# Kernel tuning notes

Hardware: AMD Instinct MI355X
Metric: run time of the kernel (lower is better)

Reference implementation:

```python
import jax, jax.numpy as jnp
import numpy as np
import math

B, S, D = 2, 2048, 2048
H, KV, HD = 32, 8, 64
G = H // KV  # 4
BASE = 10000.0


def _rope_tables(seq_len, dtype):
    inv_freq = 1.0 / (BASE ** (jnp.arange(0, HD, 2, dtype=jnp.float32) / HD))
    t = jnp.arange(seq_len, dtype=jnp.float32)
    freqs = jnp.outer(t, inv_freq)               # [S, HD/2]
    emb = jnp.concatenate([freqs, freqs], -1)     # [S, HD]
    return jnp.cos(emb).astype(dtype), jnp.sin(emb).astype(dtype)


def _rotate_half(x):
    x1, x2 = x[..., : HD // 2], x[..., HD // 2 :]
    return jnp.concatenate([-x2, x1], axis=-1)


def setup_inputs() -> dict:
    key = jax.random.key(0)
    ks = jax.random.split(key, 5)
    s = 0.02
    return {
        "hidden_states": jax.random.normal(ks[0], (B, S, D), jnp.float32),
        "Wq": jax.random.normal(ks[1], (D, H * HD), jnp.float32) * s,
        "Wk": jax.random.normal(ks[2], (D, KV * HD), jnp.float32) * s,
        "Wv": jax.random.normal(ks[3], (D, KV * HD), jnp.float32) * s,
        "Wo": jax.random.normal(ks[4], (D, D), jnp.float32) * s,
    }


def reference(hidden_states, Wq, Wk, Wv, Wo):
    b, s, _ = hidden_states.shape
    q = (hidden_states @ Wq).reshape(b, s, H, HD).transpose(0, 2, 1, 3)   # [B,H,S,HD]
    k = (hidden_states @ Wk).reshape(b, s, KV, HD).transpose(0, 2, 1, 3)  # [B,KV,S,HD]
    v = (hidden_states @ Wv).reshape(b, s, KV, HD).transpose(0, 2, 1, 3)

    cos, sin = _rope_tables(s, hidden_states.dtype)  # [S, HD]
    cos = cos[None, None]
    sin = sin[None, None]
    q = q * cos + _rotate_half(q) * sin
    k = k * cos + _rotate_half(k) * sin

    # GQA: repeat kv heads to match query heads
    k = jnp.repeat(k, G, axis=1)  # [B,H,S,HD]
    v = jnp.repeat(v, G, axis=1)

    scores = jnp.einsum("bhqd,bhkd->bhqk", q, k) / math.sqrt(HD)
    causal = jnp.triu(jnp.full((s, s), float("-inf"), dtype=scores.dtype), k=1)
    scores = scores + causal
    attn = jax.nn.softmax(scores, axis=-1)
    out = jnp.einsum("bhqk,bhkd->bhqd", attn, v)          # [B,H,S,HD]
    out = out.transpose(0, 2, 1, 3).reshape(b, s, H * HD)  # [B,S,D]
    return out @ Wo
```

## Files before the change

kernel.cpp:

```cpp
#include <hip/hip_runtime.h>
#include <hip/hip_bf16.h>

#define BATCH  2
#define SEQ    2048
#define DMODEL 2048
#define NHEADS 32
#define NKV    8
#define HDIM   64
#define ROWS   (BATCH * SEQ)
#define NQKV   3072

typedef __attribute__((ext_vector_type(8))) short bf16x8;
typedef __attribute__((ext_vector_type(4))) float floatx4;

__device__ __forceinline__ float b2f(unsigned short u) {
    union { unsigned int i; float f; } x; x.i = ((unsigned int)u) << 16; return x.f;
}
__device__ __forceinline__ unsigned short f2b(float f) {
    union { float f; unsigned int i; } x; x.f = f;
    unsigned int r = x.i + 0x7fffu + ((x.i >> 16) & 1u);
    return (unsigned short)(r >> 16);
}
__device__ __forceinline__ unsigned int pkbf(float a, float b) {
    union { __hip_bfloat162 h; unsigned int u; } x;
    x.h = __float22bfloat162_rn(make_float2(a, b));
    return x.u;
}

#define GLD16(g, l) __builtin_amdgcn_global_load_lds( \
    (const __attribute__((address_space(1))) unsigned int*)(g), \
    (__attribute__((address_space(3))) unsigned int*)(l), 16, 0, 0)

template <bool BF16_OUT>
__global__ __launch_bounds__(256) void mfma_gemm(const unsigned short* __restrict__ A,
                                                 const unsigned short* __restrict__ Bt,
                                                 void* __restrict__ Cout,
                                                 int M, int N, int K) {
    __shared__ unsigned short As[128 * 32];
    __shared__ unsigned short Bs[128 * 32];

    const int tid  = threadIdx.x;
    const int wave = tid >> 6;
    const int lane = tid & 63;
    const int m0 = blockIdx.y * 128;
    const int n0 = blockIdx.x * 128;
    const int wr0 = (wave >> 1) * 64;
    const int wc0 = (wave & 1) * 64;

    const int srow = wave * 32 + (lane >> 2);
    const int skc  = (lane & 3) * 8;
    const unsigned short* Ap0 = A  + (size_t)(m0 + srow) * K + skc;
    const unsigned short* Ap1 = Ap0 + (size_t)16 * K;
    const unsigned short* Bp0 = Bt + (size_t)(n0 + srow) * K + skc;
    const unsigned short* Bp1 = Bp0 + (size_t)16 * K;
    unsigned short* Al0 = &As[wave * 1024];
    unsigned short* Al1 = &As[wave * 1024 + 512];
    unsigned short* Bl0 = &Bs[wave * 1024];
    unsigned short* Bl1 = &Bs[wave * 1024 + 512];

    const int fr = lane & 15;
    const int fk = (lane >> 4) * 8;

    floatx4 acc[4][4];
    #pragma unroll
    for (int r = 0; r < 4; ++r)
        #pragma unroll
        for (int c = 0; c < 4; ++c)
            #pragma unroll
            for (int g = 0; g < 4; ++g) acc[r][c][g] = 0.f;

    for (int k0 = 0; k0 < K; k0 += 32) {
        __syncthreads();
        GLD16(Ap0 + k0, Al0);
        GLD16(Ap1 + k0, Al1);
        GLD16(Bp0 + k0, Bl0);
        GLD16(Bp1 + k0, Bl1);
        __syncthreads();

        bf16x8 af[4], bfr[4];
        #pragma unroll
        for (int r = 0; r < 4; ++r)
            af[r] = *(const bf16x8*)&As[(wr0 + r * 16 + fr) * 32 + fk];
        #pragma unroll
        for (int c = 0; c < 4; ++c)
            bfr[c] = *(const bf16x8*)&Bs[(wc0 + c * 16 + fr) * 32 + fk];
        #pragma unroll
        for (int r = 0; r < 4; ++r)
            #pragma unroll
            for (int c = 0; c < 4; ++c)
                acc[r][c] = __builtin_amdgcn_mfma_f32_16x16x32_bf16(af[r], bfr[c], acc[r][c], 0, 0, 0);
    }

    const int erow = (lane >> 4) * 4;
    const int ecol = lane & 15;
    #pragma unroll
    for (int r = 0; r < 4; ++r)
        #pragma unroll
        for (int c = 0; c < 4; ++c)
            #pragma unroll
            for (int g = 0; g < 4; ++g) {
                int row = m0 + wr0 + r * 16 + erow + g;
                int col = n0 + wc0 + c * 16 + ecol;
                if (BF16_OUT)
                    ((unsigned short*)Cout)[(size_t)row * N + col] = f2b(acc[r][c][g]);
                else
                    ((float*)Cout)[(size_t)row * N + col] = acc[r][c][g];
            }
}

__global__ __launch_bounds__(256) void transpose_cast_all(const float* __restrict__ Wq,
                                                          const float* __restrict__ Wk,
                                                          const float* __restrict__ Wv,
                                                          const float* __restrict__ Wo,
                                                          unsigned short* __restrict__ Wt,
                                                          unsigned short* __restrict__ Wot) {
    __shared__ float t[32][33];
    int bx = blockIdx.x;
    const float* src; unsigned short* dst; int N, nb;
    if (bx < 64)      { src = Wq; dst = Wt;                          N = 2048; nb = bx; }
    else if (bx < 80) { src = Wk; dst = Wt + (size_t)2048 * DMODEL;  N = 512;  nb = bx - 64; }
    else if (bx < 96) { src = Wv; dst = Wt + (size_t)2560 * DMODEL;  N = 512;  nb = bx - 80; }
    else              { src = Wo; dst = Wot;                         N = 2048; nb = bx - 96; }
    const int n0 = nb * 32, k0 = blockIdx.y * 32;
    const int tx = threadIdx.x & 31, ty = threadIdx.x >> 5;
    #pragma unroll
    for (int i = 0; i < 32; i += 8)
        t[ty + i][tx] = src[(size_t)(k0 + ty + i) * N + n0 + tx];
    __syncthreads();
    #pragma unroll
    for (int i = 0; i < 32; i += 8)
        dst[(size_t)(n0 + ty + i) * DMODEL + k0 + tx] = f2b(t[tx][ty + i]);
}

__global__ void cast_f32_to_bf16(const float* __restrict__ src,
                                 unsigned short* __restrict__ dst, int n) {
    int i = (blockIdx.x * 256 + threadIdx.x) * 8;
    if (i >= n) return;
    float4 a = *(const float4*)(src + i);
    float4 b = *(const float4*)(src + i + 4);
    uint4 o;
    o.x = pkbf(a.x, a.y); o.y = pkbf(a.z, a.w);
    o.z = pkbf(b.x, b.y); o.w = pkbf(b.z, b.w);
    *(uint4*)(dst + i) = o;
}

__global__ void rope_all(unsigned short* __restrict__ buf) {
    int idx = blockIdx.x * blockDim.x + threadIdx.x;
    int i   = idx & 31;
    int tmp = idx >> 5;
    int hh  = tmp % 40;
    int row = tmp / 40;
    if (row >= ROWS) return;
    float scale = (hh < 32) ? 0.125f : 1.0f;
    int t = row & (SEQ - 1);
    float inv_freq = powf(10000.0f, -(float)i * (1.0f / 32.0f));
    float ang = (float)t * inv_freq;
    float s, c;
    sincosf(ang, &s, &c);
    unsigned short* p = buf + (size_t)row * NQKV + hh * 64 + i;
    float x1 = b2f(p[0]), x2 = b2f(p[32]);
    p[0]  = f2b((x1 * c - x2 * s) * scale);
    p[32] = f2b((x2 * c + x1 * s) * scale);
}

__global__ __launch_bounds__(256, 4) void attn_mfma(const unsigned short* __restrict__ QKV,
                                                    unsigned short* __restrict__ Ctx) {
    __shared__ unsigned short Ks[64][72];
    __shared__ unsigned short Vts[64][72];
    __shared__ unsigned short Ps[4][32][72];

    const int tid  = threadIdx.x;
    const int wave = tid >> 6;
    const int lane = tid & 63;
    const int px = blockIdx.x;
    const int h  = blockIdx.y;
    const int b  = blockIdx.z;
    const int kvh = h >> 2;

    const int fr = lane & 15;
    const int fg = lane >> 4;
    const size_t base = (size_t)(b * SEQ) * NQKV;

    const int krow = tid >> 2, kc0 = (tid & 3) * 16;
    const int vp2 = tid & 31, vh0 = (tid >> 5) * 8;
    const unsigned short* kbase = QKV + base + (size_t)krow * NQKV + 2048 + kvh * HDIM + kc0;
    const unsigned short* vbase = QKV + base + (size_t)(2 * vp2) * NQKV + 2560 + kvh * HDIM + vh0;

    #pragma unroll 1
    for (int t = 0; t < 2; ++t) {
        const int qb = (t == 0) ? (15 - px) : px;
        const int wbase = qb * 128 + wave * 32;

        bf16x8 qf[2][2];
        #pragma unroll
        for (int rg = 0; rg < 2; ++rg)
            #pragma unroll
            for (int ks = 0; ks < 2; ++ks)
                qf[rg][ks] = *(const bf16x8*)(QKV + base + (size_t)(wbase + rg * 16 + fr) * NQKV
                                              + h * HDIM + ks * 32 + fg * 8);

        float l[2];
        floatx4 acc[4][2];
        #pragma unroll
        for (int rg = 0; rg < 2; ++rg) l[rg] = 0.f;
        #pragma unroll
        for (int j2 = 0; j2 < 4; ++j2)
            #pragma unroll
            for (int rg = 0; rg < 2; ++rg)
                #pragma unroll
                for (int g = 0; g < 4; ++g) acc[j2][rg][g] = 0.f;

        const int nkb = 2 * qb + 2;

        bf16x8 kr0 = *(const bf16x8*)kbase;
        bf16x8 kr1 = *(const bf16x8*)(kbase + 8);
        bf16x8 v0  = *(const bf16x8*)vbase;
        bf16x8 v1  = *(const bf16x8*)(vbase + NQKV);

        for (int kb = 0; kb < nkb; ++kb) {
            __syncthreads();
            *(bf16x8*)&Ks[krow][kc0]     = kr0;
            *(bf16x8*)&Ks[krow][kc0 + 8] = kr1;
            #pragma unroll
            for (int j = 0; j < 8; ++j) {
                unsigned int w = (unsigned int)(unsigned short)v0[j]
                               | ((unsigned int)(unsigned short)v1[j] << 16);
                *(unsigned int*)&Vts[vh0 + j][2 * vp2] = w;
            }
            {
                int nx = (kb + 1 < nkb) ? kb + 1 : kb;
                const unsigned short* kp = kbase + (size_t)(nx * 64) * NQKV;
                const unsigned short* vp = vbase + (size_t)(nx * 64) * NQKV;
                kr0 = *(const bf16x8*)kp;
                kr1 = *(const bf16x8*)(kp + 8);
                v0  = *(const bf16x8*)vp;
                v1  = *(const bf16x8*)(vp + NQKV);
            }
            __syncthreads();

            const bool skip = (kb * 64 > wbase + 31);
            if (!skip) {
                const bool needMask = (kb * 64 + 63 > wbase);

                floatx4 sc[4][2];
                #pragma unroll
                for (int j = 0; j < 4; ++j)
                    #pragma unroll
                    for (int rg = 0; rg < 2; ++rg)
                        #pragma unroll
                        for (int g = 0; g < 4; ++g) sc[j][rg][g] = 0.f;
                #pragma unroll
                for (int ks = 0; ks < 2; ++ks) {
                    #pragma unroll
                    for (int j = 0; j < 4; ++j) {
                        bf16x8 kf = *(const bf16x8*)&Ks[j * 16 + fr][ks * 32 + fg * 8];
                        #pragma unroll
                        for (int rg = 0; rg < 2; ++rg)
                            sc[j][rg] = __builtin_amdgcn_mfma_f32_16x16x32_bf16(kf, qf[rg][ks], sc[j][rg], 0, 0, 0);
                    }
                }

                if (needMask) {
                    #pragma unroll
                    for (int rg = 0; rg < 2; ++rg) {
                        int qi = wbase + rg * 16 + fr;
                        #pragma unroll
                        for (int j = 0; j < 4; ++j)
                            #pragma unroll
                            for (int g = 0; g < 4; ++g) {
                                int kj = kb * 64 + j * 16 + fg * 4 + g;
                                if (kj > qi) sc[j][rg][g] = -1e30f;
                            }
                    }
                }

                #pragma unroll
                for (int rg = 0; rg < 2; ++rg) {
                    #pragma unroll
                    for (int j = 0; j < 4; ++j) {
                        #pragma unroll
                        for (int g = 0; g < 4; ++g) {
                            float e = __expf(sc[j][rg][g]);
                            sc[j][rg][g] = e;
                            l[rg] += e;
                        }
                        uint2 w;
                        w.x = pkbf(sc[j][rg][0], sc[j][rg][1]);
                        w.y = pkbf(sc[j][rg][2], sc[j][rg][3]);
                        *(uint2*)&Ps[wave][rg * 16 + fr][j * 16 + fg * 4] = w;
                    }
                }

                #pragma unroll
                for (int ks = 0; ks < 2; ++ks) {
                    bf16x8 pf[2];
                    #pragma unroll
                    for (int rg = 0; rg < 2; ++rg)
                        pf[rg] = *(const bf16x8*)&Ps[wave][rg * 16 + fr][ks * 32 + fg * 8];
                    #pragma unroll
                    for (int j2 = 0; j2 < 4; ++j2) {
                        bf16x8 vf = *(const bf16x8*)&Vts[j2 * 16 + fr][ks * 32 + fg * 8];
                        #pragma unroll
                        for (int rg = 0; rg < 2; ++rg)
                            acc[j2][rg] = __builtin_amdgcn_mfma_f32_16x16x32_bf16(vf, pf[rg], acc[j2][rg], 0, 0, 0);
                    }
                }
            }
        }

        #pragma unroll
        for (int rg = 0; rg < 2; ++rg) {
            float lt = l[rg];
            lt += __shfl_xor(lt, 16);
            lt += __shfl_xor(lt, 32);
            float inv = 1.0f / lt;
            int q = wbase + rg * 16 + fr;
            unsigned short* cp = Ctx + (size_t)(b * SEQ + q) * DMODEL + h * HDIM;
            #pragma unroll
            for (int j2 = 0; j2 < 4; ++j2) {
                uint2 w;
                w.x = pkbf(acc[j2][rg][0] * inv, acc[j2][rg][1] * inv);
                w.y = pkbf(acc[j2][rg][2] * inv, acc[j2][rg][3] * inv);
                *(uint2*)(cp + j2 * 16 + fg * 4) = w;
            }
        }
    }
}

extern "C" void kernel_launch(void* const* d_in, const int* in_sizes, int n_in,
                              void* d_out, int out_size, void* d_ws, size_t ws_size,
                              hipStream_t stream) {
    const float* X  = (const float*)d_in[0];
    const float* Wq = (const float*)d_in[1];
    const float* Wk = (const float*)d_in[2];
    const float* Wv = (const float*)d_in[3];
    const float* Wo = (const float*)d_in[4];
    float* out = (float*)d_out;

    unsigned short* Xb   = (unsigned short*)d_ws;
    unsigned short* Wt   = Xb + (size_t)ROWS * DMODEL;
    unsigned short* Wot  = Wt + (size_t)NQKV * DMODEL;
    unsigned short* QKVb = Wot + (size_t)DMODEL * DMODEL;
    unsigned short* Ctxb = QKVb + (size_t)ROWS * NQKV;

    cast_f32_to_bf16<<<(ROWS * DMODEL) / (8 * 256), 256, 0, stream>>>(X, Xb, ROWS * DMODEL);
    transpose_cast_all<<<dim3(160, 64), 256, 0, stream>>>(Wq, Wk, Wv, Wo, Wt, Wot);

    mfma_gemm<true><<<dim3(NQKV / 128, ROWS / 128), 256, 0, stream>>>(Xb, Wt, QKVb, ROWS, NQKV, DMODEL);

    rope_all<<<(ROWS * 40 * 32) / 256, 256, 0, stream>>>(QKVb);

    attn_mfma<<<dim3(SEQ / 256, NHEADS, BATCH), 256, 0, stream>>>(QKVb, Ctxb);

    mfma_gemm<false><<<dim3(DMODEL / 128, ROWS / 128), 256, 0, stream>>>(Ctxb, Wot, out, ROWS, DMODEL, DMODEL);
}
```

Before: 345.7 us.

## Halve attention query tile per block and add MFMA priority hints

The attention kernel now gives each wave 16 query rows instead of 32, so each block covers 64 queries. Blocks still take a mirrored pair of query tiles, and the grid doubles to SEQ/128 blocks per head. This raises block count and occupancy (launch bounds 5, smaller P scratch) and cuts register pressure. It also wraps the MFMA sections in s_setprio. The cost is that each K/V tile loaded into shared memory is reused by half as many query rows, which roughly doubles K/V global traffic and barrier count per query.

Measured after the change: 329.8 us. 1.05x faster.

```diff
diff --git a/kernel.cpp b/kernel.cpp
--- a/kernel.cpp
+++ b/kernel.cpp
@@ -163,11 +163,11 @@
     p[32] = f2b((x2 * c + x1 * s) * scale);
 }
 
-__global__ __launch_bounds__(256, 4) void attn_mfma(const unsigned short* __restrict__ QKV,
+__global__ __launch_bounds__(256, 5) void attn_mfma(const unsigned short* __restrict__ QKV,
                                                     unsigned short* __restrict__ Ctx) {
     __shared__ unsigned short Ks[64][72];
     __shared__ unsigned short Vts[64][72];
-    __shared__ unsigned short Ps[4][32][72];
+    __shared__ unsigned short Ps[4][16][72];
 
     const int tid  = threadIdx.x;
     const int wave = tid >> 6;
@@ -188,29 +188,23 @@
 
     #pragma unroll 1
     for (int t = 0; t < 2; ++t) {
-        const int qb = (t == 0) ? (15 - px) : px;
-        const int wbase = qb * 128 + wave * 32;
-
-        bf16x8 qf[2][2];
-        #pragma unroll
-        for (int rg = 0; rg < 2; ++rg)
-            #pragma unroll
-            for (int ks = 0; ks < 2; ++ks)
-                qf[rg][ks] = *(const bf16x8*)(QKV + base + (size_t)(wbase + rg * 16 + fr) * NQKV
-                                              + h * HDIM + ks * 32 + fg * 8);
-
-        float l[2];
-        floatx4 acc[4][2];
-        #pragma unroll
-        for (int rg = 0; rg < 2; ++rg) l[rg] = 0.f;
+        const int qb = (t == 0) ? (31 - px) : px;
+        const int wbase = qb * 64 + wave * 16;
+
+        bf16x8 qf[2];
+        #pragma unroll
+        for (int ks = 0; ks < 2; ++ks)
+            qf[ks] = *(const bf16x8*)(QKV + base + (size_t)(wbase + fr) * NQKV
+                                      + h * HDIM + ks * 32 + fg * 8);
+
+        float l = 0.f;
+        floatx4 acc[4];
         #pragma unroll
         for (int j2 = 0; j2 < 4; ++j2)
             #pragma unroll
-            for (int rg = 0; rg < 2; ++rg)
-                #pragma unroll
-                for (int g = 0; g < 4; ++g) acc[j2][rg][g] = 0.f;
-
-        const int nkb = 2 * qb + 2;
+            for (int g = 0; g < 4; ++g) acc[j2][g] = 0.f;
+
+        const int nkb = qb + 1;
 
         bf16x8 kr0 = *(const bf16x8*)kbase;
         bf16x8 kr1 = *(const bf16x8*)(kbase + 8);
@@ -238,89 +232,77 @@
             }
             __syncthreads();
 
-            const bool skip = (kb * 64 > wbase + 31);
+            const bool skip = (kb * 64 > wbase + 15);
             if (!skip) {
                 const bool needMask = (kb * 64 + 63 > wbase);
 
-                floatx4 sc[4][2];
+                floatx4 sc[4];
                 #pragma unroll
                 for (int j = 0; j < 4; ++j)
                     #pragma unroll
-                    for (int rg = 0; rg < 2; ++rg)
-                        #pragma unroll
-                        for (int g = 0; g < 4; ++g) sc[j][rg][g] = 0.f;
+                    for (int g = 0; g < 4; ++g) sc[j][g] = 0.f;
+                __builtin_amdgcn_s_setprio(1);
                 #pragma unroll
                 for (int ks = 0; ks < 2; ++ks) {
                     #pragma unroll
                     for (int j = 0; j < 4; ++j) {
                         bf16x8 kf = *(const bf16x8*)&Ks[j * 16 + fr][ks * 32 + fg * 8];
-                        #pragma unroll
-                        for (int rg = 0; rg < 2; ++rg)
-                            sc[j][rg] = __builtin_amdgcn_mfma_f32_16x16x32_bf16(kf, qf[rg][ks], sc[j][rg], 0, 0, 0);
+                        sc[j] = __builtin_amdgcn_mfma_f32_16x16x32_bf16(kf, qf[ks], sc[j], 0, 0, 0);
                     }
                 }
+                __builtin_amdgcn_s_setprio(0);
 
                 if (needMask) {
-                    #pragma unroll
-                    for (int rg = 0; rg < 2; ++rg) {
-                        int qi = wbase + rg * 16 + fr;
+                    int qi = wbase + fr;
+                    #pragma unroll
+                    for (int j = 0; j < 4; ++j)
                         #pragma unroll
-                        for (int j = 0; j < 4; ++j)
-                            #pragma unroll
-                            for (int g = 0; g < 4; ++g) {
-                                int kj = kb * 64 + j * 16 + fg * 4 + g;
-                                if (kj > qi) sc[j][rg][g] = -1e30f;
-                            }
+                        for (int g = 0; g < 4; ++g) {
+                            int kj = kb * 64 + j * 16 + fg * 4 + g;
+                            if (kj > qi) sc[j][g] = -1e30f;
+                        }
+                }
+
+                #pragma unroll
+                for (int j = 0; j < 4; ++j) {
+                    #pragma unroll
+                    for (int g = 0; g < 4; ++g) {
+                        float e = __expf(sc[j][g]);
+                        sc[j][g] = e;
+                        l += e;
+                    }
+                    uint2 w;
+                    w.x = pkbf(sc[j][0], sc[j][1]);
+                    w.y = pkbf(sc[j][2], sc[j][3]);
+                    *(uint2*)&Ps[wave][fr][j * 16 + fg * 4] = w;
+                }
+
+                __builtin_amdgcn_s_setprio(1);
+                #pragma unroll
+                for (int ks = 0; ks < 2; ++ks) {
+                    bf16x8 pf = *(const bf16x8*)&Ps[wave][fr][ks * 32 + fg * 8];
+                    #pragma unroll
+                    for (int j2 = 0; j2 < 4; ++j2) {
+                        bf16x8 vf = *(const bf16x8*)&Vts[j2 * 16 + fr][ks * 32 + fg * 8];
+                        acc[j2] = __builtin_amdgcn_mfma_f32_16x16x32_bf16(vf, pf, acc[j2], 0, 0, 0);
                     }
                 }
-
-                #pragma unroll
-                for (int rg = 0; rg < 2; ++rg) {
-                    #pragma unroll
-                    for (int j = 0; j < 4; ++j) {
-                        #pragma unroll
-                        for (int g = 0; g < 4; ++g) {
-                            float e = __expf(sc[j][rg][g]);
-                            sc[j][rg][g] = e;
-                            l[rg] += e;
-                        }
-                        uint2 w;
-                        w.x = pkbf(sc[j][rg][0], sc[j][rg][1]);
-                        w.y = pkbf(sc[j][rg][2], sc[j][rg][3]);
-                        *(uint2*)&Ps[wave][rg * 16 + fr][j * 16 + fg * 4] = w;
-                    }
-                }
-
-                #pragma unroll
-                for (int ks = 0; ks < 2; ++ks) {
-                    bf16x8 pf[2];
-                    #pragma unroll
-                    for (int rg = 0; rg < 2; ++rg)
-                        pf[rg] = *(const bf16x8*)&Ps[wave][rg * 16 + fr][ks * 32 + fg * 8];
-                    #pragma unroll
-                    for (int j2 = 0; j2 < 4; ++j2) {
-                        bf16x8 vf = *(const bf16x8*)&Vts[j2 * 16 + fr][ks * 32 + fg * 8];
-                        #pragma unroll
-                        for (int rg = 0; rg < 2; ++rg)
-                            acc[j2][rg] = __builtin_amdgcn_mfma_f32_16x16x32_bf16(vf, pf[rg], acc[j2][rg], 0, 0, 0);
-                    }
-                }
+                __builtin_amdgcn_s_setprio(0);
             }
         }
 
-        #pragma unroll
-        for (int rg = 0; rg < 2; ++rg) {
-            float lt = l[rg];
+        {
+            float lt = l;
             lt += __shfl_xor(lt, 16);
             lt += __shfl_xor(lt, 32);
             float inv = 1.0f / lt;
-            int q = wbase + rg * 16 + fr;
+            int q = wbase + fr;
             unsigned short* cp = Ctx + (size_t)(b * SEQ + q) * DMODEL + h * HDIM;
             #pragma unroll
             for (int j2 = 0; j2 < 4; ++j2) {
                 uint2 w;
-                w.x = pkbf(acc[j2][rg][0] * inv, acc[j2][rg][1] * inv);
-                w.y = pkbf(acc[j2][rg][2] * inv, acc[j2][rg][3] * inv);
+                w.x = pkbf(acc[j2][0] * inv, acc[j2][1] * inv);
+                w.y = pkbf(acc[j2][2] * inv, acc[j2][3] * inv);
                 *(uint2*)(cp + j2 * 16 + fg * 4) = w;
             }
         }
@@ -350,7 +332,7 @@
 
     rope_all<<<(ROWS * 40 * 32) / 256, 256, 0, stream>>>(QKVb);
 
-    attn_mfma<<<dim3(SEQ / 256, NHEADS, BATCH), 256, 0, stream>>>(QKVb, Ctxb);
+    attn_mfma<<<dim3(SEQ / 128, NHEADS, BATCH), 256, 0, stream>>>(QKVb, Ctxb);
 
     mfma_gemm<false><<<dim3(DMODEL / 128, ROWS / 128), 256, 0, stream>>>(Ctxb, Wot, out, ROWS, DMODEL, DMODEL);
 }
```
